# Optimization experiments

Hardware: AMD Instinct MI355X
Metric: run time of the kernel (lower is better)

## Reference

```python
import jax, jax.numpy as jnp
import numpy as np


def _adj(M):
    # conjugate transpose of the last two (color) dims
    return jnp.conj(jnp.swapaxes(M, -1, -2))


def _plaquettes(U):
    # U: (B, L1..Ld, d, Nc, Nc) complex -> (B, L1..Ld, d*(d-1)/2, Nc, Nc)
    d = U.shape[-3]
    plaqs = []
    for mu in range(d):
        for nu in range(mu + 1, d):
            U_mu = U[..., mu, :, :]
            U_nu = U[..., nu, :, :]
            U_mu_fwd = jnp.roll(U_mu, -1, axis=1 + nu)
            U_nu_fwd = jnp.roll(U_nu, -1, axis=1 + mu)
            plaqs.append(U_mu @ U_nu_fwd @ _adj(U_mu_fwd) @ _adj(U_nu))
    return jnp.stack(plaqs, axis=-3)


def _polyakov(U):
    # Poly[..., mu] = U_mu(x) @ U_mu(x+mu) @ ... @ U_mu(x+(L_mu-1)mu)
    d = U.shape[-3]
    lattice_shape = U.shape[1:-3]
    loops = []
    for mu in range(d):
        U_mu = U[..., mu, :, :]
        P = U_mu
        shifted = U_mu
        for _ in range(1, lattice_shape[mu]):
            shifted = jnp.roll(shifted, -1, axis=1 + mu)
            P = P @ shifted
        loops.append(P)
    return jnp.stack(loops, axis=-3)


def setup_inputs() -> dict:
    key = jax.random.key(0)
    ks = jax.random.split(key, 4)
    B, L, d, Nc = 2, 16, 4, 3
    N_out, N_in, K = 8, 10, 1
    shapeU = (B, L, L, L, L, d, Nc, Nc)
    return {
        "U_re": jax.random.normal(ks[0], shapeU, jnp.float32),
        "U_im": jax.random.normal(ks[1], shapeU, jnp.float32),
        "omega_re": jax.random.normal(ks[2], (N_out, N_in, d, 2 * K + 1), jnp.float32),
        "omega_im": jax.random.normal(ks[3], (N_out, N_in, d, 2 * K + 1), jnp.float32),
        "K": K,
        "N_out": N_out,
    }


def reference(U_re, U_im, omega_re, omega_im, K, N_out):
    U = U_re + 1j * U_im            # complex64 gauge links (B, L1..L4, d, Nc, Nc)
    omega = omega_re + 1j * omega_im  # (N_out, N_in, d, 2K+1)
    d = U.shape[-3]

    # W = locally transforming variables: plaquettes + Polyakov loops, N_in channels
    W = jnp.concatenate([_plaquettes(U), _polyakov(U)], axis=-3)

    # NOTE: the original torch get_ParallelTransporters never writes the cumulative
    # products back into the tensor (in-place bug), so the transporters used by
    # L_conv are exactly U_mu for every shift k. We reproduce that behavior.
    W_conv = jnp.zeros(U.shape[:-3] + (N_out,) + U.shape[-2:], dtype=U.dtype)
    for k in range(-K, K + 1):
        i_k = k + K
        for mu in range(d):
            W_sh = jnp.roll(W, -k, axis=1 + mu)      # (B, lat, N_in, Nc, Nc)
            A = U[..., mu, :, :]                      # effective transporter (B, lat, Nc, Nc)
            W_conv = W_conv + jnp.einsum(
                'ij,...ac,...jcd,...db->...iab',
                omega[..., mu, i_k], A, W_sh, _adj(A), optimize=True)
    return W_conv
```

## Files before the change

kernel.cpp:

```cpp
#include <hip/hip_runtime.h>

#define LSZ   16
#define NBATCH 2
#define NSITE (NBATCH*LSZ*LSZ*LSZ*LSZ)
#define NIN   10
#define NOUT  8
#define ND    4
#define NCPLX ((long)NSITE * NOUT * 9)
#define NLINE_PER_DIR (NSITE / LSZ)
#define NLINK (NSITE * ND)
#define WSTRIDE 108

typedef unsigned int u32;
typedef float  f32x4 __attribute__((ext_vector_type(4)));
typedef short  s16x8 __attribute__((ext_vector_type(8)));

struct M3 { float re[9]; float im[9]; };

__device__ __forceinline__ unsigned short f2bf(float x) {
    u32 u = __float_as_uint(x);
    u32 r = (u + 0x7fffu + ((u >> 16) & 1u)) >> 16;
    return (unsigned short)r;
}
__device__ __forceinline__ u32 packbf(float lo, float hi) {
    return (u32)f2bf(lo) | ((u32)f2bf(hi) << 16);
}

__device__ __forceinline__ s16x8 as_s16x8(uint4 v) {
    union { uint4 u; s16x8 s; } x; x.u = v; return x.s;
}

__device__ __forceinline__ void mulM(M3& o, const M3& a, const M3& b) {
#pragma unroll
    for (int r = 0; r < 3; r++) {
#pragma unroll
        for (int c = 0; c < 3; c++) {
            float xr = 0.f, xi = 0.f;
#pragma unroll
            for (int k = 0; k < 3; k++) {
                float ar = a.re[r*3+k], ai = a.im[r*3+k];
                float br = b.re[k*3+c], bi = b.im[k*3+c];
                xr = fmaf(ar, br, xr); xr = fmaf(-ai, bi, xr);
                xi = fmaf(ar, bi, xi); xi = fmaf(ai, br, xi);
            }
            o.re[r*3+c] = xr; o.im[r*3+c] = xi;
        }
    }
}

__device__ __forceinline__ void mulAdjM(M3& o, const M3& a, const M3& b) {
#pragma unroll
    for (int r = 0; r < 3; r++) {
#pragma unroll
        for (int c = 0; c < 3; c++) {
            float xr = 0.f, xi = 0.f;
#pragma unroll
            for (int k = 0; k < 3; k++) {
                float ar = a.re[r*3+k], ai = a.im[r*3+k];
                float br = b.re[c*3+k], bi = b.im[c*3+k];
                xr = fmaf(ar, br, xr); xr = fmaf(ai, bi, xr);
                xi = fmaf(ai, br, xi); xi = fmaf(-ar, bi, xi);
            }
            o.re[r*3+c] = xr; o.im[r*3+c] = xi;
        }
    }
}

__device__ __forceinline__ int shift_site(int s, int mu, int k) {
    int sh = 12 - 4 * mu;
    int c  = (s >> sh) & 15;
    int nc = (c + k) & 15;
    return (s & ~(15 << sh)) | (nc << sh);
}

__global__ __launch_bounds__(256) void poly_kernel(const float* __restrict__ Ure,
                                                   const float* __restrict__ Uim,
                                                   u32* __restrict__ T2) {
    __shared__ float2 sm[16 * 145];

    int line0 = blockIdx.x * 16;
    int mu    = line0 / NLINE_PER_DIR;
    int lidx0 = line0 - mu * NLINE_PER_DIR;
    int sh    = 12 - 4 * mu;
    int low0  = lidx0 & ((1 << sh) - 1);
    int high0 = lidx0 >> sh;
    int s_base0 = (high0 << (sh + 4)) | low0;

    for (int n = threadIdx.x; n < 16 * 16 * 9; n += 256) {
        int siteIdx = n / 9;
        int e       = n - siteIdx * 9;
        int site, l, c;
        if (mu == 3) { site = (lidx0 << 4) + siteIdx; l = siteIdx >> 4; c = siteIdx & 15; }
        else         { site = s_base0 + ((siteIdx >> 4) << sh) + (siteIdx & 15);
                       l = siteIdx & 15; c = siteIdx >> 4; }
        long g = ((long)site * 4 + mu) * 9 + e;
        sm[l * 145 + c * 9 + e] = make_float2(Ure[g], Uim[g]);
    }
    __syncthreads();

    int c = threadIdx.x & 15;
    int l = threadIdx.x >> 4;

    M3 P;
    {
        const float2* m0 = &sm[l * 145 + c * 9];
#pragma unroll
        for (int e = 0; e < 9; e++) { float2 v = m0[e]; P.re[e] = v.x; P.im[e] = v.y; }
    }
    for (int step = 1; step < LSZ; step++) {
        const float2* mn = &sm[l * 145 + ((c + step) & 15) * 9];
        M3 Un, Tm;
#pragma unroll
        for (int e = 0; e < 9; e++) { float2 v = mn[e]; Un.re[e] = v.x; Un.im[e] = v.y; }
        mulM(Tm, P, Un);
        P = Tm;
    }

    int lidx = lidx0 + l;
    int low  = lidx & ((1 << sh) - 1);
    int high = lidx >> sh;
    int site = (high << (sh + 4)) | (c << sh) | low;
    u32* Tp = T2 + ((long)site * 4 + mu) * 9;
#pragma unroll
    for (int e = 0; e < 9; e++) Tp[e] = packbf(P.re[e], P.im[e]);
}

__global__ __launch_bounds__(192) void plaq_merge_kernel(const float* __restrict__ Ure,
                                                         const float* __restrict__ Uim,
                                                         const u32* __restrict__ T2,
                                                         u32* __restrict__ W) {
    __shared__ __align__(16) char smem[4 * 32 * 37 * sizeof(float2)];
    float2* sU = (float2*)smem;
    u32*    sw = (u32*)smem;

    int s0 = blockIdx.x * 32;

    for (int n = threadIdx.x; n < 8 * 16 * 36; n += 192) {
        int run = n / 576;
        int q   = n - run * 576;
        int sir = q / 36;
        int e36 = q - sir * 36;
        int slot = run >> 1, r = run & 1;
        int base = s0 + r * 16;
        if (slot < 3) base = shift_site(base, slot, 1);
        long g = (long)(base + sir) * 36 + e36;
        sU[(slot * 32 + r * 16 + sir) * 37 + e36] = make_float2(Ure[g], Uim[g]);
    }
    __syncthreads();

    int p  = threadIdx.x >> 5;
    int ls = threadIdx.x & 31;

    int mu = (p < 3) ? 0 : ((p < 5) ? 1 : 2);
    int nu = (mu == 0) ? (p + 1) : ((mu == 1) ? (p - 1) : 3);

    M3 Umu, Unu, Unu_f, Umu_f, T1, T2m, P;
    {
        const float2* pp;
#define LDM(m, slot, site, link) \
        pp = &sU[((slot) * 32 + (site)) * 37 + (link) * 9]; \
        _Pragma("unroll") \
        for (int e = 0; e < 9; e++) { float2 v = pp[e]; (m).re[e] = v.x; (m).im[e] = v.y; }

        LDM(Umu, 3, ls, mu);
        LDM(Unu, 3, ls, nu);
        LDM(Unu_f, mu, ls, nu);
        int lsrot = (ls & 16) | ((ls + 1) & 15);
        int fslot = (nu == 3) ? 3 : nu;
        int fsite = (nu == 3) ? lsrot : ls;
        LDM(Umu_f, fslot, fsite, mu);
#undef LDM
    }

    mulM(T1, Umu, Unu_f);
    mulAdjM(T2m, T1, Umu_f);
    mulAdjM(P, T2m, Unu);

    __syncthreads();

#pragma unroll
    for (int e = 0; e < 9; e++) sw[ls * WSTRIDE + e * 12 + p] = packbf(P.re[e], P.im[e]);

    for (int it = threadIdx.x; it < 32 * 9 * 2; it += 192) {
        int site = it / 18;
        int r    = it - site * 18;
        sw[site * WSTRIDE + (r >> 1) * 12 + 10 + (r & 1)] = 0u;
    }

    for (int it = threadIdx.x; it < 32 * 36; it += 192) {
        int ls2 = it / 36;
        int r   = it - ls2 * 36;
        int mu2 = r / 9;
        int e2  = r - mu2 * 9;
        sw[ls2 * WSTRIDE + e2 * 12 + 6 + mu2] = T2[(long)(s0 + ls2) * 36 + r];
    }
    __syncthreads();

    uint4* W4 = (uint4*)W;
    for (int it = threadIdx.x; it < 27 * 32; it += 192) {
        int pl  = it >> 5;
        int ls2 = it & 31;
        int e   = pl / 3, q = pl - e * 3;
        const uint4 v = *(const uint4*)(sw + ls2 * WSTRIDE + e * 12 + q * 4);
        W4[(long)pl * NSITE + s0 + ls2] = v;
    }
}

template <int MODE>
__global__ __launch_bounds__(256) void conv_kernel(const float* __restrict__ Ure,
                                                   const float* __restrict__ Uim,
                                                   const u32* __restrict__ W,
                                                   const float* __restrict__ omre,
                                                   const float* __restrict__ omim,
                                                   float* __restrict__ out) {
    __shared__ __align__(16) char smraw[64 * 72 * sizeof(float)];
    uint4* somB = (uint4*)smraw;
    float* sout = (float*)smraw;

    for (int n = threadIdx.x; n < 12 * 64; n += 256) {
        int mk = n >> 6, ln = n & 63;
        int q = ln >> 4, c = ln & 15, i = c & 7;
        int mu = mk / 3, kk = mk - mu * 3;
        u32 wv[4];
#pragma unroll
        for (int w = 0; w < 4; w++) {
            int j = q * 4 + w;
            u32 val = 0u;
            if (q < 3 && j < NIN) {
                int oidx = ((i * NIN + j) * ND + mu) * 3 + kk;
                float orv = omre[oidx], oiv = omim[oidx];
                val = (c < 8) ? packbf(orv, -oiv) : packbf(oiv, orv);
            }
            wv[w] = val;
        }
        somB[n] = make_uint4(wv[0], wv[1], wv[2], wv[3]);
    }
    __syncthreads();

    int chunk = gridDim.x >> 3;
    int lb    = ((int)blockIdx.x & 7) * chunk + ((int)blockIdx.x >> 3);

    int lane = threadIdx.x & 63;
    int wv_  = threadIdx.x >> 6;
    int r    = lane & 15;
    int q    = lane >> 4;
    int s0b  = lb * 64;
    int sline = s0b + wv_ * 16;

    const uint4* W4 = (const uint4*)W;

    bool hi = (r >= 8);
    int  i  = r & 7;
    int  reg0 = hi ? 2 : 0;

    float accr[2][9], acci[2][9];
#pragma unroll
    for (int rr = 0; rr < 2; rr++)
#pragma unroll
        for (int e = 0; e < 9; e++) { accr[rr][e] = 0.f; acci[rr][e] = 0.f; }

    for (int mu = 0; mu < ND; mu++) {
        f32x4 acc[9];
#pragma unroll
        for (int e = 0; e < 9; e++) acc[e] = (f32x4)(0.f);

        for (int kk = 0; kk < 3; kk++) {
            int mk = mu * 3 + kk;
            s16x8 bfrag = as_s16x8(somB[mk * 64 + lane]);

            int nb;
            if (mu < 3) nb = shift_site(sline, mu, kk - 1) + r;
            else        nb = sline + ((r + kk - 1) & 15);

            uint4 w9[9];
            if (q < 3) {
#pragma unroll
                for (int e = 0; e < 9; e++) w9[e] = W4[(long)(e * 3 + q) * NSITE + nb];
            } else {
#pragma unroll
                for (int e = 0; e < 9; e++) w9[e] = make_uint4(0u, 0u, 0u, 0u);
            }
#pragma unroll
            for (int e = 0; e < 9; e++)
                acc[e] = __builtin_amdgcn_mfma_f32_16x16x32_bf16(as_s16x8(w9[e]), bfrag, acc[e], 0, 0, 0);
        }

        float own[2][9], oth[2][9];
#pragma unroll
        for (int e = 0; e < 9; e++) {
            float t0 = __shfl_xor(acc[e][0], 8);
            float t1 = __shfl_xor(acc[e][1], 8);
            float t2 = __shfl_xor(acc[e][2], 8);
            float t3 = __shfl_xor(acc[e][3], 8);
            own[0][e] = hi ? acc[e][2] : acc[e][0];
            own[1][e] = hi ? acc[e][3] : acc[e][1];
            oth[0][e] = hi ? t2 : t0;
            oth[1][e] = hi ? t3 : t1;
        }

#pragma unroll
        for (int rr = 0; rr < 2; rr++) {
            int site = sline + q * 4 + reg0 + rr;
            M3 A, M;
            {
                const float* pr = Ure + ((long)site * 4 + mu) * 9;
                const float* pi = Uim + ((long)site * 4 + mu) * 9;
#pragma unroll
                for (int e = 0; e < 9; e++) { A.re[e] = pr[e]; A.im[e] = pi[e]; }
            }
#pragma unroll
            for (int e = 0; e < 9; e++) {
                M.re[e] = hi ? oth[rr][e] : own[rr][e];
                M.im[e] = hi ? own[rr][e] : oth[rr][e];
            }
            M3 Tm;
#pragma unroll
            for (int rw = 0; rw < 3; rw++) {
#pragma unroll
                for (int cl = 0; cl < 3; cl++) {
                    float xr = 0.f, xi = 0.f;
#pragma unroll
                    for (int k = 0; k < 3; k++) {
                        float ar = A.re[rw*3+k], ai = A.im[rw*3+k];
                        float br = M.re[k*3+cl], bi = M.im[k*3+cl];
                        xr = fmaf(ar, br, xr); xr = fmaf(-ai, bi, xr);
                        xi = fmaf(ar, bi, xi); xi = fmaf(ai, br, xi);
                    }
                    Tm.re[rw*3+cl] = xr; Tm.im[rw*3+cl] = xi;
                }
            }
#pragma unroll
            for (int rw = 0; rw < 3; rw++) {
#pragma unroll
                for (int cl = 0; cl < 3; cl++) {
                    float xr = 0.f, xi = 0.f;
#pragma unroll
                    for (int k = 0; k < 3; k++) {
                        float ar = Tm.re[rw*3+k], ai = Tm.im[rw*3+k];
                        float br = A.re[cl*3+k], bi = A.im[cl*3+k];
                        xr = fmaf(ar, br, xr); xr = fmaf(ai, bi, xr);
                        if (MODE != 2) { xi = fmaf(ai, br, xi); xi = fmaf(-ar, bi, xi); }
                    }
                    accr[rr][rw*3+cl] += xr;
                    if (MODE != 2) acci[rr][rw*3+cl] += xi;
                }
            }
        }
    }

    if (MODE == 2) {
        __syncthreads();
#pragma unroll
        for (int rr = 0; rr < 2; rr++) {
            int tloc = wv_ * 16 + q * 4 + reg0 + rr;
#pragma unroll
            for (int e = 0; e < 9; e++)
                sout[(tloc * 8 + i) * 9 + e] = accr[rr][e];
        }
        __syncthreads();
        long base = (long)lb * 4608;
        for (int n = threadIdx.x; n < 4608; n += 256) out[base + n] = sout[n];
    } else if (MODE == 0) {
#pragma unroll
        for (int rr = 0; rr < 2; rr++) {
            int site = sline + q * 4 + reg0 + rr;
            long cb = ((long)site * 8 + i) * 9;
            float2* op = (float2*)(out + cb * 2);
#pragma unroll
            for (int e = 0; e < 9; e++) op[e] = make_float2(accr[rr][e], acci[rr][e]);
        }
    } else {
#pragma unroll
        for (int rr = 0; rr < 2; rr++) {
            int site = sline + q * 4 + reg0 + rr;
            long cb = ((long)site * 8 + i) * 9;
#pragma unroll
            for (int e = 0; e < 9; e++) {
                out[cb + e]         = accr[rr][e];
                out[NCPLX + cb + e] = acci[rr][e];
            }
        }
    }
}

extern "C" void kernel_launch(void* const* d_in, const int* in_sizes, int n_in,
                              void* d_out, int out_size, void* d_ws, size_t ws_size,
                              hipStream_t stream) {
    const float* Ure  = (const float*)d_in[0];
    const float* Uim  = (const float*)d_in[1];
    const float* omre = (const float*)d_in[2];
    const float* omim = (const float*)d_in[3];
    float* out = (float*)d_out;

    const size_t wBytes = (size_t)NSITE * WSTRIDE * sizeof(u32);
    if (ws_size < wBytes) return;

    u32* W  = (u32*)d_ws;
    u32* T2 = (u32*)d_out;

    poly_kernel<<<NSITE * 4 / (16 * 16), 256, 0, stream>>>(Ure, Uim, T2);
    plaq_merge_kernel<<<NSITE / 32, 192, 0, stream>>>(Ure, Uim, T2, W);

    const int convGrid = NSITE / 64;
    if (out_size == (int)NCPLX)
        conv_kernel<2><<<convGrid, 256, 0, stream>>>(Ure, Uim, W, omre, omim, out);
    else if (out_size == (int)(2 * NCPLX))
        conv_kernel<1><<<convGrid, 256, 0, stream>>>(Ure, Uim, W, omre, omim, out);
    else
        conv_kernel<0><<<convGrid, 256, 0, stream>>>(Ure, Uim, W, omre, omim, out);
}
```

Before: 255.0 us.

## Compute Polyakov loops by log-depth shuffle doubling and prefetch T2 loads

The Polyakov kernel drops the shared-memory staging and the 15-step serial chain of matrix products. Each lane instead loads its own link and does 4 rounds of recursive doubling, using wave shuffles to fetch the product held by the lane k positions ahead, so only 4 complex 3x3 multiplies run per site. In the plaquette kernel the T2 loads are issued up front into registers, so their latency overlaps the link staging and the plaquette math. Global loads in the Polyakov kernel become strided per lane instead of coalesced through shared memory, and register pressure rises from the prefetched values.

```diff
diff --git a/kernel.cpp b/kernel.cpp
--- a/kernel.cpp
+++ b/kernel.cpp
@@ -76,51 +76,37 @@
 __global__ __launch_bounds__(256) void poly_kernel(const float* __restrict__ Ure,
                                                    const float* __restrict__ Uim,
                                                    u32* __restrict__ T2) {
-    __shared__ float2 sm[16 * 145];
-
-    int line0 = blockIdx.x * 16;
-    int mu    = line0 / NLINE_PER_DIR;
-    int lidx0 = line0 - mu * NLINE_PER_DIR;
-    int sh    = 12 - 4 * mu;
-    int low0  = lidx0 & ((1 << sh) - 1);
-    int high0 = lidx0 >> sh;
-    int s_base0 = (high0 << (sh + 4)) | low0;
-
-    for (int n = threadIdx.x; n < 16 * 16 * 9; n += 256) {
-        int siteIdx = n / 9;
-        int e       = n - siteIdx * 9;
-        int site, l, c;
-        if (mu == 3) { site = (lidx0 << 4) + siteIdx; l = siteIdx >> 4; c = siteIdx & 15; }
-        else         { site = s_base0 + ((siteIdx >> 4) << sh) + (siteIdx & 15);
-                       l = siteIdx & 15; c = siteIdx >> 4; }
-        long g = ((long)site * 4 + mu) * 9 + e;
-        sm[l * 145 + c * 9 + e] = make_float2(Ure[g], Uim[g]);
-    }
-    __syncthreads();
-
-    int c = threadIdx.x & 15;
-    int l = threadIdx.x >> 4;
-
-    M3 P;
-    {
-        const float2* m0 = &sm[l * 145 + c * 9];
-#pragma unroll
-        for (int e = 0; e < 9; e++) { float2 v = m0[e]; P.re[e] = v.x; P.im[e] = v.y; }
-    }
-    for (int step = 1; step < LSZ; step++) {
-        const float2* mn = &sm[l * 145 + ((c + step) & 15) * 9];
-        M3 Un, Tm;
-#pragma unroll
-        for (int e = 0; e < 9; e++) { float2 v = mn[e]; Un.re[e] = v.x; Un.im[e] = v.y; }
-        mulM(Tm, P, Un);
-        P = Tm;
-    }
-
-    int lidx = lidx0 + l;
+    int lane = threadIdx.x & 63;
+    int c    = lane & 15;
+    int l    = lane >> 4;
+    int wv   = threadIdx.x >> 6;
+    int lineG = blockIdx.x * 16 + wv * 4 + l;
+    int mu   = lineG / NLINE_PER_DIR;
+    int lidx = lineG - mu * NLINE_PER_DIR;
+    int sh   = 12 - 4 * mu;
     int low  = lidx & ((1 << sh) - 1);
     int high = lidx >> sh;
     int site = (high << (sh + 4)) | (c << sh) | low;
-    u32* Tp = T2 + ((long)site * 4 + mu) * 9;
+    long base = ((long)site * 4 + mu) * 9;
+
+    M3 P;
+#pragma unroll
+    for (int e = 0; e < 9; e++) { P.re[e] = Ure[base + e]; P.im[e] = Uim[base + e]; }
+
+#pragma unroll
+    for (int k = 1; k < 16; k <<= 1) {
+        int src = (lane & 48) | ((c + k) & 15);
+        M3 Q, T;
+#pragma unroll
+        for (int e = 0; e < 9; e++) {
+            Q.re[e] = __shfl(P.re[e], src);
+            Q.im[e] = __shfl(P.im[e], src);
+        }
+        mulM(T, P, Q);
+        P = T;
+    }
+
+    u32* Tp = T2 + base;
 #pragma unroll
     for (int e = 0; e < 9; e++) Tp[e] = packbf(P.re[e], P.im[e]);
 }
@@ -134,6 +120,18 @@
     u32*    sw = (u32*)smem;
 
     int s0 = blockIdx.x * 32;
+
+    u32 tpre[6]; int tofs[6];
+#pragma unroll
+    for (int w = 0; w < 6; w++) {
+        int it = threadIdx.x + w * 192;
+        tpre[w] = T2[(long)s0 * 36 + it];
+        int ls2 = it / 36;
+        int r   = it - ls2 * 36;
+        int mu2 = r / 9;
+        int e2  = r - mu2 * 9;
+        tofs[w] = ls2 * WSTRIDE + e2 * 12 + 6 + mu2;
+    }
 
     for (int n = threadIdx.x; n < 8 * 16 * 36; n += 192) {
         int run = n / 576;
@@ -187,13 +185,8 @@
         sw[site * WSTRIDE + (r >> 1) * 12 + 10 + (r & 1)] = 0u;
     }
 
-    for (int it = threadIdx.x; it < 32 * 36; it += 192) {
-        int ls2 = it / 36;
-        int r   = it - ls2 * 36;
-        int mu2 = r / 9;
-        int e2  = r - mu2 * 9;
-        sw[ls2 * WSTRIDE + e2 * 12 + 6 + mu2] = T2[(long)(s0 + ls2) * 36 + r];
-    }
+#pragma unroll
+    for (int w = 0; w < 6; w++) sw[tofs[w]] = tpre[w];
     __syncthreads();
 
     uint4* W4 = (uint4*)W;
```

Result: faster. 239.8 us (-6.0%).

## Stage conv links in LDS, doubling-shuffle Polyakov product, prefetch T2 loads

Applied to the files above, without the earlier changes.

The conv kernel now copies each block's 64 sites of gauge links into shared memory with coalesced loads. Each thread then reads its transporter matrix from shared memory instead of issuing strided global reads inside the mu loop. This grows the kernel's shared memory allocation, which may lower occupancy. The Polyakov kernel replaces its 15 serial 3x3 complex multiplies with 4 doubling steps that exchange partial cyclic products across lanes with shuffles. The plaquette-merge kernel issues its T2 global loads into registers at kernel start so they overlap the U staging.

```diff
diff --git a/kernel.cpp b/kernel.cpp
--- a/kernel.cpp
+++ b/kernel.cpp
@@ -98,8 +98,9 @@
     }
     __syncthreads();
 
-    int c = threadIdx.x & 15;
-    int l = threadIdx.x >> 4;
+    int lane = threadIdx.x & 63;
+    int c    = threadIdx.x & 15;
+    int l    = threadIdx.x >> 4;
 
     M3 P;
     {
@@ -107,13 +108,18 @@
 #pragma unroll
         for (int e = 0; e < 9; e++) { float2 v = m0[e]; P.re[e] = v.x; P.im[e] = v.y; }
     }
-    for (int step = 1; step < LSZ; step++) {
-        const float2* mn = &sm[l * 145 + ((c + step) & 15) * 9];
-        M3 Un, Tm;
-#pragma unroll
-        for (int e = 0; e < 9; e++) { float2 v = mn[e]; Un.re[e] = v.x; Un.im[e] = v.y; }
-        mulM(Tm, P, Un);
-        P = Tm;
+
+#pragma unroll
+    for (int k = 1; k < 16; k <<= 1) {
+        int src = (lane & 48) | ((c + k) & 15);
+        M3 Q, T;
+#pragma unroll
+        for (int e = 0; e < 9; e++) {
+            Q.re[e] = __shfl(P.re[e], src);
+            Q.im[e] = __shfl(P.im[e], src);
+        }
+        mulM(T, P, Q);
+        P = T;
     }
 
     int lidx = lidx0 + l;
@@ -134,6 +140,18 @@
     u32*    sw = (u32*)smem;
 
     int s0 = blockIdx.x * 32;
+
+    u32 tpre[6]; int tofs[6];
+#pragma unroll
+    for (int w = 0; w < 6; w++) {
+        int it = threadIdx.x + w * 192;
+        tpre[w] = T2[(long)s0 * 36 + it];
+        int ls2 = it / 36;
+        int r   = it - ls2 * 36;
+        int mu2 = r / 9;
+        int e2  = r - mu2 * 9;
+        tofs[w] = ls2 * WSTRIDE + e2 * 12 + 6 + mu2;
+    }
 
     for (int n = threadIdx.x; n < 8 * 16 * 36; n += 192) {
         int run = n / 576;
@@ -187,13 +205,8 @@
         sw[site * WSTRIDE + (r >> 1) * 12 + 10 + (r & 1)] = 0u;
     }
 
-    for (int it = threadIdx.x; it < 32 * 36; it += 192) {
-        int ls2 = it / 36;
-        int r   = it - ls2 * 36;
-        int mu2 = r / 9;
-        int e2  = r - mu2 * 9;
-        sw[ls2 * WSTRIDE + e2 * 12 + 6 + mu2] = T2[(long)(s0 + ls2) * 36 + r];
-    }
+#pragma unroll
+    for (int w = 0; w < 6; w++) sw[tofs[w]] = tpre[w];
     __syncthreads();
 
     uint4* W4 = (uint4*)W;
@@ -213,9 +226,10 @@
                                                    const float* __restrict__ omre,
                                                    const float* __restrict__ omim,
                                                    float* __restrict__ out) {
-    __shared__ __align__(16) char smraw[64 * 72 * sizeof(float)];
-    uint4* somB = (uint4*)smraw;
-    float* sout = (float*)smraw;
+    __shared__ __align__(16) char smraw[12288 + 18432];
+    uint4*  somB = (uint4*)smraw;
+    float2* sU   = (float2*)(smraw + 12288);
+    float*  sout = (float*)(smraw + 12288);
 
     for (int n = threadIdx.x; n < 12 * 64; n += 256) {
         int mk = n >> 6, ln = n & 63;
@@ -235,16 +249,21 @@
         }
         somB[n] = make_uint4(wv[0], wv[1], wv[2], wv[3]);
     }
-    __syncthreads();
 
     int chunk = gridDim.x >> 3;
     int lb    = ((int)blockIdx.x & 7) * chunk + ((int)blockIdx.x >> 3);
+    int s0b   = lb * 64;
+
+    for (int n = threadIdx.x; n < 64 * 36; n += 256) {
+        long g = (long)s0b * 36 + n;
+        sU[n] = make_float2(Ure[g], Uim[g]);
+    }
+    __syncthreads();
 
     int lane = threadIdx.x & 63;
     int wv_  = threadIdx.x >> 6;
     int r    = lane & 15;
     int q    = lane >> 4;
-    int s0b  = lb * 64;
     int sline = s0b + wv_ * 16;
 
     const uint4* W4 = (const uint4*)W;
@@ -300,13 +319,12 @@
 
 #pragma unroll
         for (int rr = 0; rr < 2; rr++) {
-            int site = sline + q * 4 + reg0 + rr;
+            int siteLoc = wv_ * 16 + q * 4 + reg0 + rr;
             M3 A, M;
             {
-                const float* pr = Ure + ((long)site * 4 + mu) * 9;
-                const float* pi = Uim + ((long)site * 4 + mu) * 9;
-#pragma unroll
-                for (int e = 0; e < 9; e++) { A.re[e] = pr[e]; A.im[e] = pi[e]; }
+                const float2* pA = sU + siteLoc * 36 + mu * 9;
+#pragma unroll
+                for (int e = 0; e < 9; e++) { float2 v = pA[e]; A.re[e] = v.x; A.im[e] = v.y; }
             }
 #pragma unroll
             for (int e = 0; e < 9; e++) {
```

Result: faster. 239.7 us (-6.0%).
